# Performance work log

Measured on AMD Instinct MI355X. Metric: run time of the kernel, lower is better.

Reference implementation:

```python
import jax, jax.numpy as jnp
import numpy as np

L = 6      # layers (enc and dec)
D = 512    # d_model
H = 8      # heads
DK = D // H
F = 2048   # dim_feedforward
B = 8
S = 512    # src len
T = 512    # tgt len
NEG = -1e9


def setup_inputs() -> dict:
    key = jax.random.key(0)
    ks = jax.random.split(key, 64)
    it = iter(ks)
    def w(shape, scale=0.02):
        return jax.random.normal(next(it), shape, dtype=jnp.float32) * scale
    inp = {}
    inp['src'] = jax.random.normal(next(it), (B, S, D), dtype=jnp.float32)
    inp['tgt'] = jax.random.normal(next(it), (B, T, D), dtype=jnp.float32)
    inp['tgt_mask'] = jnp.where(jnp.triu(jnp.ones((T, T), bool), 1), jnp.float32(NEG), jnp.float32(0.0))
    # encoder params (stacked over L layers)
    inp['enc_Wq'] = w((L, H, D, DK)); inp['enc_Wk'] = w((L, H, D, DK)); inp['enc_Wv'] = w((L, H, D, DK))
    inp['enc_Wo'] = w((L, D, D))
    inp['enc_ln1_a'] = jnp.ones((L, D)); inp['enc_ln1_b'] = jnp.zeros((L, D))
    inp['enc_W1'] = w((L, D, F)); inp['enc_b1'] = jnp.zeros((L, F))
    inp['enc_W2'] = w((L, F, D)); inp['enc_b2'] = jnp.zeros((L, D))
    inp['enc_ln2_a'] = jnp.ones((L, D)); inp['enc_ln2_b'] = jnp.zeros((L, D))
    # decoder params
    inp['dec_sWq'] = w((L, H, D, DK)); inp['dec_sWk'] = w((L, H, D, DK)); inp['dec_sWv'] = w((L, H, D, DK))
    inp['dec_sWo'] = w((L, D, D))
    inp['dec_ln1_a'] = jnp.ones((L, D)); inp['dec_ln1_b'] = jnp.zeros((L, D))
    inp['dec_cWq'] = w((L, H, D, DK)); inp['dec_cWk'] = w((L, H, D, DK)); inp['dec_cWv'] = w((L, H, D, DK))
    inp['dec_cWo'] = w((L, D, D))
    inp['dec_ln2_a'] = jnp.ones((L, D)); inp['dec_ln2_b'] = jnp.zeros((L, D))
    inp['dec_W1'] = w((L, D, F)); inp['dec_b1'] = jnp.zeros((L, F))
    inp['dec_W2'] = w((L, F, D)); inp['dec_b2'] = jnp.zeros((L, D))
    inp['dec_ln3_a'] = jnp.ones((L, D)); inp['dec_ln3_b'] = jnp.zeros((L, D))
    return inp


def layernorm(x, a, b):
    # faithful to the torch module: unbiased std (ddof=1) and eps added to std
    mean = x.mean(-1, keepdims=True)
    std = jnp.std(x, axis=-1, keepdims=True, ddof=1)
    return a * (x - mean) / (std + 1e-6) + b


def mha(qx, kx, vx, Wq, Wk, Wv, Wo, mask):
    # Wq/Wk/Wv: [H, D, dk] (per-head torch loop fused into one batched einsum)
    q = jnp.einsum('bsd,hdk->bhsk', qx, Wq)
    k = jnp.einsum('bsd,hdk->bhsk', kx, Wk)
    v = jnp.einsum('bsd,hdk->bhsk', vx, Wv)
    scores = jnp.einsum('bhqk,bhmk->bhqm', q, k) / np.float32(np.sqrt(Wq.shape[-1]))
    if mask is not None:
        scores = scores + mask  # [T,T] broadcasts over batch and heads
    attn = jax.nn.softmax(scores, axis=-1)
    o = jnp.einsum('bhqm,bhmk->bhqk', attn, v)
    b_, h_, s_, k_ = o.shape
    o = o.transpose(0, 2, 1, 3).reshape(b_, s_, h_ * k_)  # concat heads
    return o @ Wo


def ffn(x, W1, b1, W2, b2):
    return jnp.maximum(x @ W1 + b1, 0.0) @ W2 + b2


def reference(src, tgt, tgt_mask,
              enc_Wq, enc_Wk, enc_Wv, enc_Wo, enc_ln1_a, enc_ln1_b,
              enc_W1, enc_b1, enc_W2, enc_b2, enc_ln2_a, enc_ln2_b,
              dec_sWq, dec_sWk, dec_sWv, dec_sWo, dec_ln1_a, dec_ln1_b,
              dec_cWq, dec_cWk, dec_cWv, dec_cWo, dec_ln2_a, dec_ln2_b,
              dec_W1, dec_b1, dec_W2, dec_b2, dec_ln3_a, dec_ln3_b):
    # encoder
    x = src
    for i in range(L):
        h = x + mha(x, x, x, enc_Wq[i], enc_Wk[i], enc_Wv[i], enc_Wo[i], None)
        x = layernorm(h, enc_ln1_a[i], enc_ln1_b[i])
        h = x + ffn(x, enc_W1[i], enc_b1[i], enc_W2[i], enc_b2[i])
        x = layernorm(h, enc_ln2_a[i], enc_ln2_b[i])
    memory = x
    # decoder
    y = tgt
    for i in range(L):
        h = y + mha(y, y, y, dec_sWq[i], dec_sWk[i], dec_sWv[i], dec_sWo[i], tgt_mask)
        y = layernorm(h, dec_ln1_a[i], dec_ln1_b[i])
        h = y + mha(y, memory, memory, dec_cWq[i], dec_cWk[i], dec_cWv[i], dec_cWo[i], None)
        y = layernorm(h, dec_ln2_a[i], dec_ln2_b[i])
        h = y + ffn(y, dec_W1[i], dec_b1[i], dec_W2[i], dec_b2[i])
        y = layernorm(h, dec_ln3_a[i], dec_ln3_b[i])
    return y
```

## Files before the change

### kernel.cpp

```cpp
#include <hip/hip_runtime.h>
#include <hip/hip_bf16.h>

typedef unsigned short u16;
typedef __hip_bfloat16 hbf;
typedef __bf16 bf16x8 __attribute__((ext_vector_type(8)));
typedef float f32x4 __attribute__((ext_vector_type(4)));

#define LL 6
#define DD 512
#define HH 8
#define DKK 64
#define FF 2048
#define BB 8
#define SS 512

#define GLL(gp, lp)                                                        \
  __builtin_amdgcn_global_load_lds(                                        \
      (const __attribute__((address_space(1))) void*)(gp),                 \
      (__attribute__((address_space(3))) void*)(lp), 16, 0, 0)

__global__ __launch_bounds__(256) void cvt_k(const float* __restrict__ x,
                                             hbf* __restrict__ y, int n) {
  for (int i = (blockIdx.x * 256 + threadIdx.x) * 4; i < n; i += gridDim.x * 1024) {
    float4 v = *(const float4*)(x + i);
    y[i] = __float2bfloat16(v.x);
    y[i + 1] = __float2bfloat16(v.y);
    y[i + 2] = __float2bfloat16(v.z);
    y[i + 3] = __float2bfloat16(v.w);
  }
}

__global__ __launch_bounds__(256) void transpose_k(const float* __restrict__ src,
                                                   hbf* __restrict__ dst, int R, int C) {
  __shared__ hbf tile[64][65];
  const int b = blockIdx.z;
  src += (size_t)b * R * C;
  dst += (size_t)b * R * C;
  int c0 = blockIdx.x * 64, r0 = blockIdx.y * 64;
  int tx = threadIdx.x & 63;
  int ty = threadIdx.x >> 6;
#pragma unroll
  for (int i = 0; i < 16; i++) {
    int r = ty + i * 4;
    tile[r][tx] = __float2bfloat16(src[(size_t)(r0 + r) * C + c0 + tx]);
  }
  __syncthreads();
#pragma unroll
  for (int i = 0; i < 16; i++) {
    int r = ty + i * 4;
    dst[(size_t)(c0 + r) * R + r0 + tx] = tile[tx][r];
  }
}

__global__ __launch_bounds__(256) void transpose_qkv_k(const float* __restrict__ Wq,
                                                       const float* __restrict__ Wk,
                                                       const float* __restrict__ Wv,
                                                       hbf* __restrict__ dst) {
  __shared__ hbf tile[64][65];
  const int z = blockIdx.z;
  const int l = z / 24, r = z - l * 24;
  const int zw = r >> 3, h = r & 7;
  const float* src =
      (zw == 0 ? Wq : (zw == 1 ? Wk : Wv)) + ((size_t)l * HH + h) * DD * DKK;
  const int r0 = blockIdx.y * 64;
  const int tx = threadIdx.x & 63, ty = threadIdx.x >> 6;
#pragma unroll
  for (int i = 0; i < 16; i++) {
    int rr = ty + i * 4;
    tile[rr][tx] = __float2bfloat16(src[(size_t)(r0 + rr) * DKK + tx]);
  }
  __syncthreads();
  hbf* d = dst + (size_t)l * 3 * DD * DD + ((size_t)zw * 512 + h * 64) * DD + r0;
#pragma unroll
  for (int i = 0; i < 16; i++) {
    int rr = ty + i * 4;
    d[(size_t)rr * DD + tx] = tile[tx][rr];
  }
}

template <int BM, int MODE, int SPLITK>
__global__ __launch_bounds__(128) void gemm_nt(
    const u16* __restrict__ A, const u16* __restrict__ Bm, void* __restrict__ Cout,
    void* __restrict__ C2, void* __restrict__ C3,
    const float* __restrict__ bias, const hbf* __restrict__ res,
    int M, int N, int K, int lda, int ldb, int ldc, int ncoloff,
    long sAo, long sAi, long sBo, long sBi, long sCo, long sCi, int inner, float scale,
    const u16* __restrict__ A2) {
  constexpr int BN = 64, BK = 64;
  constexpr int AM = BM / 32;
  constexpr int NCA = BM / 16;
  constexpr int WR = BM / 2;
  __shared__ u16 As[2][BM * BK];
  __shared__ u16 Bs[2][BN * BK];

  int bxx = blockIdx.x, byy = blockIdx.y;
  {
    const int gx = gridDim.x, gy = gridDim.y;
    const int f = byy * gx + bxx;
    const int st = gy >> 3;
    const int rem = f >> 3;
    byy = (f & 7) * st + rem % st;
    bxx = rem / st;
  }

  int g = blockIdx.z;
  int ks = 0;
  if (SPLITK > 1) {
    ks = g;
    g = 0;
  }
  int outer = g / inner, inr = g - outer * inner;
  A += outer * sAo + inr * sAi;
  Bm += outer * sBo + inr * sBi;

  const int tid = threadIdx.x;
  const int m0 = byy * BM, n0 = (bxx + ncoloff) * BN;
  const int wave = tid >> 6, lane = tid & 63;
  const int m16 = lane & 15, quad = lane >> 4;
  const int l8 = lane & 7, ld8 = lane >> 3;
  const int scol = (l8 ^ ld8) << 3;

  const u16* Asel = (MODE == 4 && n0 >= 512) ? A2 : A;
  const u16* Ab = Asel + (size_t)m0 * lda;
  const u16* Bb = Bm + (size_t)n0 * ldb;

  f32x4 acc[AM][4] = {};

  const int kbeg = ks * (K / SPLITK);
  const int nt = (K / SPLITK) / BK;

  auto stage = [&](int b, int k0) {
#pragma unroll
    for (int c = 0; c < NCA; c++) {
      const int ch = wave * NCA + c;
      const int row = ch * 8 + ld8;
      GLL(Ab + (size_t)row * lda + k0 + scol, &As[b][ch * 512]);
    }
#pragma unroll
    for (int c = 0; c < 4; c++) {
      const int ch = wave * 4 + c;
      const int row = ch * 8 + ld8;
      GLL(Bb + (size_t)row * ldb + k0 + scol, &Bs[b][ch * 512]);
    }
  };

  stage(0, kbeg);
  __syncthreads();
  for (int t = 0; t < nt; t++) {
    if (t + 1 < nt) stage((t + 1) & 1, kbeg + (t + 1) * BK);
    const int cb = t & 1;
#pragma unroll
    for (int kc = 0; kc < 2; kc++) {
      bf16x8 af[AM], bfv[4];
      const int sw = (((kc << 2) | quad) ^ (m16 & 7)) << 3;
#pragma unroll
      for (int i = 0; i < AM; i++)
        af[i] = *(const bf16x8*)(&As[cb][(wave * WR + i * 16 + m16) * 64 + sw]);
#pragma unroll
      for (int j = 0; j < 4; j++)
        bfv[j] = *(const bf16x8*)(&Bs[cb][(j * 16 + m16) * 64 + sw]);
#pragma unroll
      for (int i = 0; i < AM; i++)
#pragma unroll
        for (int j = 0; j < 4; j++)
          acc[i][j] = __builtin_amdgcn_mfma_f32_16x16x32_bf16(af[i], bfv[j], acc[i][j], 0, 0, 0);
    }
    __syncthreads();
  }

#pragma unroll
  for (int i = 0; i < AM; i++) {
#pragma unroll
    for (int j = 0; j < 4; j++) {
      const int col = n0 + j * 16 + m16;
      const int rowb = m0 + wave * WR + i * 16 + quad * 4;
#pragma unroll
      for (int r = 0; r < 4; r++) {
        const int row = rowb + r;
        float v = acc[i][j][r] * scale;
        if (MODE == 0) {
          hbf* C = (hbf*)Cout + outer * sCo + inr * sCi;
          C[(size_t)row * ldc + col] = __float2bfloat16(v);
        } else if (MODE == 2) {
          float* C = (float*)((SPLITK > 1 && ks == 1) ? C2 : Cout);
          C += outer * sCo + inr * sCi;
          if (SPLITK == 1 || ks == 0) {
            if (bias) v += bias[col];
            if (res) v += __bfloat162float(res[(size_t)row * ldc + col]);
          }
          C[(size_t)row * ldc + col] = v;
        } else if (MODE == 3) {
          hbf* C = (hbf*)Cout + outer * sCo + inr * sCi;
          v += bias[col];
          C[(size_t)row * ldc + col] = __float2bfloat16(fmaxf(v, 0.0f));
        } else if (MODE == 4) {
          const int b = row >> 9, s = row & 511;
          const int which = col >> 9, h = (col >> 6) & 7, dk = col & 63;
          const int bh = (b << 3) + h;
          if (which == 0)
            ((hbf*)Cout)[((size_t)bh * SS + s) * DKK + dk] = __float2bfloat16(v * 0.125f);
          else if (which == 1)
            ((hbf*)C2)[((size_t)bh * SS + s) * DKK + dk] = __float2bfloat16(v);
          else
            ((hbf*)C3)[((size_t)bh * DKK + dk) * SS + s] = __float2bfloat16(v);
        }
      }
    }
  }
}

__global__ __launch_bounds__(256) void flash_k(const u16* __restrict__ Q,
                                               const u16* __restrict__ Kb,
                                               const u16* __restrict__ Vt,
                                               hbf* __restrict__ O, int causal) {
  __shared__ u16 Qs[32][72];
  __shared__ u16 Ks[128 * 72];
  __shared__ u16 Ss[32][520];
  const int bh = blockIdx.y;
  const int q0 = blockIdx.x * 32;
  const int b = bh >> 3, h = bh & 7;
  const int tid = threadIdx.x;
  const int wave = tid >> 6, lane = tid & 63;
  const int m16 = lane & 15, quad = lane >> 4;
  const int rg = (wave >> 1) * 16;
  const int chf = wave & 1;

  const u16* Qp = Q + ((size_t)bh * SS + q0) * DKK;
  const u16* Kp = Kb + (size_t)bh * SS * DKK;
  const u16* Vp = Vt + (size_t)bh * DKK * SS;

  const int ktmax = causal ? ((q0 + 31) >> 7) + 1 : 4;

  {
    int row = tid >> 3, ch = (tid & 7) << 3;
    *(float4*)(&Qs[row][ch]) = *(const float4*)(Qp + (size_t)row * DKK + ch);
  }

  for (int kt = 0; kt < ktmax; kt++) {
    if (kt > 0) __syncthreads();
#pragma unroll
    for (int p = 0; p < 4; p++) {
      int idx = p * 256 + tid;
      int row = idx >> 3, ch = (idx & 7) << 3;
      *(float4*)(&Ks[row * 72 + ch]) =
          *(const float4*)(Kp + (size_t)(kt * 128 + row) * DKK + ch);
    }
    __syncthreads();
#pragma unroll
    for (int ct = 0; ct < 4; ct++) {
      f32x4 s{};
#pragma unroll
      for (int kc = 0; kc < 2; kc++) {
        bf16x8 a = *(const bf16x8*)(&Qs[rg + m16][kc * 32 + quad * 8]);
        bf16x8 bv =
            *(const bf16x8*)(&Ks[(chf * 64 + ct * 16 + m16) * 72 + kc * 32 + quad * 8]);
        s = __builtin_amdgcn_mfma_f32_16x16x32_bf16(a, bv, s, 0, 0, 0);
      }
      const int colb = kt * 128 + chf * 64 + ct * 16 + m16;
#pragma unroll
      for (int r = 0; r < 4; r++)
        *((hbf*)&Ss[rg + quad * 4 + r][colb]) = __float2bfloat16(s[r]);
    }
  }
  __syncthreads();

#pragma unroll
  for (int rr = 0; rr < 8; rr++) {
    const int r = wave * 8 + rr;
    const int gr = q0 + r;
    float v[8];
#pragma unroll
    for (int i = 0; i < 8; i++) {
      const int col = lane + i * 64;
      v[i] = __bfloat162float(((const hbf*)Ss[r])[col]);
      if (causal && col > gr) v[i] = -1e30f;
    }
    float m = v[0];
#pragma unroll
    for (int i = 1; i < 8; i++) m = fmaxf(m, v[i]);
#pragma unroll
    for (int off = 1; off < 64; off <<= 1) m = fmaxf(m, __shfl_xor(m, off));
    float e[8], s = 0.f;
#pragma unroll
    for (int i = 0; i < 8; i++) {
      e[i] = __expf(v[i] - m);
      s += e[i];
    }
#pragma unroll
    for (int off = 1; off < 64; off <<= 1) s += __shfl_xor(s, off);
    const float inv = 1.0f / s;
#pragma unroll
    for (int i = 0; i < 8; i++)
      ((hbf*)Ss[r])[lane + i * 64] = __float2bfloat16(e[i] * inv);
  }
  __syncthreads();

  f32x4 o[2] = {};
  u16* Vs = Ks;
  for (int vt = 0; vt < ktmax; vt++) {
    if (vt > 0) __syncthreads();
#pragma unroll
    for (int p = 0; p < 4; p++) {
      int idx = p * 256 + tid;
      int row = idx >> 4, ch = (idx & 15) << 3;
      *(float4*)(&Vs[row * 136 + ch]) =
          *(const float4*)(Vp + (size_t)row * SS + vt * 128 + ch);
    }
    __syncthreads();
#pragma unroll
    for (int kc = 0; kc < 4; kc++) {
      bf16x8 a = *(const bf16x8*)(&Ss[rg + m16][vt * 128 + kc * 32 + quad * 8]);
#pragma unroll
      for (int dt = 0; dt < 2; dt++) {
        bf16x8 bv =
            *(const bf16x8*)(&Vs[(chf * 32 + dt * 16 + m16) * 136 + kc * 32 + quad * 8]);
        o[dt] = __builtin_amdgcn_mfma_f32_16x16x32_bf16(a, bv, o[dt], 0, 0, 0);
      }
    }
  }
#pragma unroll
  for (int dt = 0; dt < 2; dt++) {
    const int d = h * 64 + chf * 32 + dt * 16 + m16;
#pragma unroll
    for (int r = 0; r < 4; r++) {
      const int row = q0 + rg + quad * 4 + r;
      O[(size_t)b * SS * DD + (size_t)row * DD + d] = __float2bfloat16(o[dt][r]);
    }
  }
}

template <typename T>
__global__ __launch_bounds__(256) void layernorm_k(const float* __restrict__ X,
                                                   const float* __restrict__ X2,
                                                   const float* __restrict__ ga,
                                                   const float* __restrict__ gb,
                                                   T* __restrict__ out, int Dn) {
  const int row = blockIdx.x;
  X += (size_t)row * Dn;
  X2 += (size_t)row * Dn;
  out += (size_t)row * Dn;
  const int t = threadIdx.x;
  float2 xv = *(const float2*)(X + 2 * t);
  float2 x2 = *(const float2*)(X2 + 2 * t);
  xv.x += x2.x;
  xv.y += x2.y;
  float s = xv.x + xv.y, ss = xv.x * xv.x + xv.y * xv.y;
#pragma unroll
  for (int off = 32; off > 0; off >>= 1) {
    s += __shfl_down(s, off);
    ss += __shfl_down(ss, off);
  }
  __shared__ float sm[8];
  __shared__ float smean, sinv;
  const int wv = t >> 6, ln = t & 63;
  if (ln == 0) {
    sm[wv] = s;
    sm[4 + wv] = ss;
  }
  __syncthreads();
  if (t == 0) {
    float S1 = sm[0] + sm[1] + sm[2] + sm[3];
    float S2 = sm[4] + sm[5] + sm[6] + sm[7];
    float mean = S1 / Dn;
    float var = (S2 - S1 * mean) / (Dn - 1);
    var = fmaxf(var, 0.0f);
    smean = mean;
    sinv = 1.0f / (sqrtf(var) + 1e-6f);
  }
  __syncthreads();
  const float mean = smean, inv = sinv;
  float o0 = ga[2 * t] * (xv.x - mean) * inv + gb[2 * t];
  float o1 = ga[2 * t + 1] * (xv.y - mean) * inv + gb[2 * t + 1];
  if constexpr (sizeof(T) == 2) {
    out[2 * t] = (T)__float2bfloat16(o0);
    out[2 * t + 1] = (T)__float2bfloat16(o1);
  } else {
    out[2 * t] = o0;
    out[2 * t + 1] = o1;
  }
}

extern "C" void kernel_launch(void* const* d_in, const int* in_sizes, int n_in,
                              void* d_out, int out_size, void* d_ws, size_t ws_size,
                              hipStream_t stream) {
  (void)in_sizes; (void)n_in; (void)out_size;
  const float* src = (const float*)d_in[0];
  const float* tgt = (const float*)d_in[1];
  const float* eWq = (const float*)d_in[3];
  const float* eWk = (const float*)d_in[4];
  const float* eWv = (const float*)d_in[5];
  const float* eWo = (const float*)d_in[6];
  const float* eln1a = (const float*)d_in[7];
  const float* eln1b = (const float*)d_in[8];
  const float* eW1 = (const float*)d_in[9];
  const float* eb1 = (const float*)d_in[10];
  const float* eW2 = (const float*)d_in[11];
  const float* eb2 = (const float*)d_in[12];
  const float* eln2a = (const float*)d_in[13];
  const float* eln2b = (const float*)d_in[14];
  const float* sWq = (const float*)d_in[15];
  const float* sWk = (const float*)d_in[16];
  const float* sWv = (const float*)d_in[17];
  const float* sWo = (const float*)d_in[18];
  const float* dln1a = (const float*)d_in[19];
  const float* dln1b = (const float*)d_in[20];
  const float* cWq = (const float*)d_in[21];
  const float* cWk = (const float*)d_in[22];
  const float* cWv = (const float*)d_in[23];
  const float* cWo = (const float*)d_in[24];
  const float* dln2a = (const float*)d_in[25];
  const float* dln2b = (const float*)d_in[26];
  const float* dW1 = (const float*)d_in[27];
  const float* db1 = (const float*)d_in[28];
  const float* dW2 = (const float*)d_in[29];
  const float* db2 = (const float*)d_in[30];
  const float* dln3a = (const float*)d_in[31];
  const float* dln3b = (const float*)d_in[32];

  const size_t MB = 1024 * 1024;
  char* ws = (char*)d_ws;
  const size_t QKV_L = (size_t)3 * DD * DD;
  const size_t WO_L = (size_t)DD * DD;
  const size_t WF_L = (size_t)DD * FF;
  const bool preT = ws_size >= 150 * MB;

  hbf *qkvT_all = nullptr, *woT_all = nullptr, *w1T_all = nullptr, *w2T_all = nullptr;
  hbf *wqkvS = nullptr, *woS = nullptr, *w1S = nullptr, *w2S = nullptr;
  char* actb;
  if (preT) {
    qkvT_all = (hbf*)(ws);
    woT_all = (hbf*)(ws + 28311552);
    w1T_all = (hbf*)(ws + 37748736);
    w2T_all = (hbf*)(ws + 62914560);
    actb = ws + 84 * MB;
  } else {
    if (ws_size < 72 * MB) return;
    wqkvS = (hbf*)(ws);
    woS = (hbf*)(ws + 2 * MB);
    w1S = (hbf*)(ws + 2 * MB + 512 * 1024);
    w2S = (hbf*)(ws + 4 * MB + 512 * 1024);
    actb = ws + 7 * MB;
  }
  hbf* sbuf = (hbf*)(actb);
  u16* xbuf = (u16*)(actb + 4 * MB);
  hbf* tbuf = (hbf*)(actb + 8 * MB);
  u16* ybuf = (u16*)(actb + 12 * MB);
  u16* qbuf = (u16*)(actb + 16 * MB);
  u16* kbuf = (u16*)(actb + 20 * MB);
  u16* vtb = (u16*)(actb + 24 * MB);
  u16* obuf = (u16*)(actb + 28 * MB);
  u16* ffnh = (u16*)(actb + 32 * MB);
  float* projf = (float*)(actb + 48 * MB);
  float* projf2 = (float*)(actb + 56 * MB);

  const size_t WQL = (size_t)HH * DD * DKK;
  const size_t WOL = (size_t)DD * DD;
  const size_t WFL = (size_t)DD * FF;

  if (preT) {
    transpose_qkv_k<<<dim3(1, 8, LL * 24), dim3(256), 0, stream>>>(eWq, eWk, eWv, qkvT_all);
    transpose_qkv_k<<<dim3(1, 8, LL * 24), dim3(256), 0, stream>>>(sWq, sWk, sWv,
                                                                   qkvT_all + LL * QKV_L);
    transpose_qkv_k<<<dim3(1, 8, LL * 24), dim3(256), 0, stream>>>(
        cWq, cWk, cWv, qkvT_all + 2 * LL * QKV_L);
    transpose_k<<<dim3(8, 8, LL), dim3(256), 0, stream>>>(eWo, woT_all, DD, DD);
    transpose_k<<<dim3(8, 8, LL), dim3(256), 0, stream>>>(sWo, woT_all + LL * WO_L, DD, DD);
    transpose_k<<<dim3(8, 8, LL), dim3(256), 0, stream>>>(cWo, woT_all + 2 * LL * WO_L, DD, DD);
    transpose_k<<<dim3(32, 8, LL), dim3(256), 0, stream>>>(eW1, w1T_all, DD, FF);
    transpose_k<<<dim3(32, 8, LL), dim3(256), 0, stream>>>(dW1, w1T_all + LL * WF_L, DD, FF);
    transpose_k<<<dim3(8, 32, LL), dim3(256), 0, stream>>>(eW2, w2T_all, FF, DD);
    transpose_k<<<dim3(8, 32, LL), dim3(256), 0, stream>>>(dW2, w2T_all + LL * WF_L, FF, DD);
  }

  auto attention = [&](const u16* qin, const u16* kvin, const hbf* qkvTl, const hbf* woTl,
                       const u16* resid, int causal) {
    gemm_nt<128, 4, 1><<<dim3(24, 32, 1), dim3(128), 0, stream>>>(
        qin, (const u16*)qkvTl, qbuf, kbuf, vtb, nullptr, nullptr,
        BB * SS, 3 * DD, DD, DD, DD, 0, 0,
        0, 0, 0, 0, 0, 0, 1, 1.f, kvin);
    flash_k<<<dim3(16, 64), dim3(256), 0, stream>>>(qbuf, kbuf, vtb, (hbf*)obuf, causal);
    gemm_nt<64, 2, 2><<<dim3(8, 64, 2), dim3(128), 0, stream>>>(
        obuf, (const u16*)woTl, projf, projf2, nullptr, nullptr, (const hbf*)resid,
        BB * SS, DD, DD, DD, DD, DD, 0,
        0, 0, 0, 0, 0, 0, 1, 1.f, nullptr);
  };

  auto ffn = [&](const u16* xin, const hbf* w1Tl, const float* b1l, const hbf* w2Tl,
                 const float* b2l) {
    gemm_nt<128, 3, 1><<<dim3(32, 32, 1), dim3(128), 0, stream>>>(
        xin, (const u16*)w1Tl, ffnh, nullptr, nullptr, b1l, nullptr,
        BB * SS, FF, DD, DD, DD, FF, 0,
        0, 0, 0, 0, 0, 0, 1, 1.f, nullptr);
    gemm_nt<64, 2, 2><<<dim3(8, 64, 2), dim3(128), 0, stream>>>(
        ffnh, (const u16*)w2Tl, projf, projf2, nullptr, b2l, (const hbf*)xin,
        BB * SS, DD, FF, FF, FF, DD, 0,
        0, 0, 0, 0, 0, 0, 1, 1.f, nullptr);
  };

  auto lnb = [&](const float* X, const float* a, const float* b, u16* out) {
    layernorm_k<hbf><<<dim3(BB * SS), dim3(256), 0, stream>>>(X, projf2, a, b, (hbf*)out, DD);
  };

  cvt_k<<<dim3(2048), dim3(256), 0, stream>>>(src, sbuf, BB * SS * DD);
  cvt_k<<<dim3(2048), dim3(256), 0, stream>>>(tgt, tbuf, BB * SS * DD);

  const u16* cur = (const u16*)sbuf;
  for (int l = 0; l < LL; l++) {
    const hbf *qkvTl, *woTl, *w1Tl, *w2Tl;
    if (preT) {
      qkvTl = qkvT_all + (size_t)l * QKV_L;
      woTl = woT_all + (size_t)l * WO_L;
      w1Tl = w1T_all + (size_t)l * WF_L;
      w2Tl = w2T_all + (size_t)l * WF_L;
    } else {
      transpose_qkv_k<<<dim3(1, 8, 24), dim3(256), 0, stream>>>(
          eWq + l * WQL, eWk + l * WQL, eWv + l * WQL, wqkvS);
      transpose_k<<<dim3(8, 8, 1), dim3(256), 0, stream>>>(eWo + l * WOL, woS, DD, DD);
      qkvTl = wqkvS;
      woTl = woS;
    }
    attention(cur, cur, qkvTl, woTl, cur, 0);
    lnb(projf, eln1a + l * DD, eln1b + l * DD, xbuf);
    if (!preT) {
      transpose_k<<<dim3(32, 8, 1), dim3(256), 0, stream>>>(eW1 + l * WFL, w1S, DD, FF);
      transpose_k<<<dim3(8, 32, 1), dim3(256), 0, stream>>>(eW2 + l * WFL, w2S, FF, DD);
      w1Tl = w1S;
      w2Tl = w2S;
    }
    ffn(xbuf, w1Tl, eb1 + l * FF, w2Tl, eb2 + l * DD);
    lnb(projf, eln2a + l * DD, eln2b + l * DD, xbuf);
    cur = xbuf;
  }
  const u16* mem = cur;
  const u16* yc = (const u16*)tbuf;
  for (int l = 0; l < LL; l++) {
    const hbf *sqkvTl, *swoTl, *cqkvTl, *cwoTl, *w1Tl, *w2Tl;
    if (preT) {
      sqkvTl = qkvT_all + ((size_t)LL + l) * QKV_L;
      swoTl = woT_all + ((size_t)LL + l) * WO_L;
      cqkvTl = qkvT_all + ((size_t)2 * LL + l) * QKV_L;
      cwoTl = woT_all + ((size_t)2 * LL + l) * WO_L;
      w1Tl = w1T_all + ((size_t)LL + l) * WF_L;
      w2Tl = w2T_all + ((size_t)LL + l) * WF_L;
    }
    if (!preT) {
      transpose_qkv_k<<<dim3(1, 8, 24), dim3(256), 0, stream>>>(
          sWq + l * WQL, sWk + l * WQL, sWv + l * WQL, wqkvS);
      transpose_k<<<dim3(8, 8, 1), dim3(256), 0, stream>>>(sWo + l * WOL, woS, DD, DD);
      sqkvTl = wqkvS;
      swoTl = woS;
    }
    attention(yc, yc, sqkvTl, swoTl, yc, 1);
    lnb(projf, dln1a + l * DD, dln1b + l * DD, ybuf);
    yc = ybuf;
    if (!preT) {
      transpose_qkv_k<<<dim3(1, 8, 24), dim3(256), 0, stream>>>(
          cWq + l * WQL, cWk + l * WQL, cWv + l * WQL, wqkvS);
      transpose_k<<<dim3(8, 8, 1), dim3(256), 0, stream>>>(cWo + l * WOL, woS, DD, DD);
      cqkvTl = wqkvS;
      cwoTl = woS;
    }
    attention(yc, mem, cqkvTl, cwoTl, yc, 0);
    lnb(projf, dln2a + l * DD, dln2b + l * DD, ybuf);
    if (!preT) {
      transpose_k<<<dim3(32, 8, 1), dim3(256), 0, stream>>>(dW1 + l * WFL, w1S, DD, FF);
      transpose_k<<<dim3(8, 32, 1), dim3(256), 0, stream>>>(dW2 + l * WFL, w2S, FF, DD);
      w1Tl = w1S;
      w2Tl = w2S;
    }
    ffn(ybuf, w1Tl, db1 + l * FF, w2Tl, db2 + l * DD);
    if (l == LL - 1) {
      layernorm_k<float><<<dim3(BB * SS), dim3(256), 0, stream>>>(
          projf, projf2, dln3a + l * DD, dln3b + l * DD, (float*)d_out, DD);
    } else {
      lnb(projf, dln3a + l * DD, dln3b + l * DD, ybuf);
      yc = ybuf;
    }
  }
}
```

Measured before the change: 2.112 ms.

## Fuse output-projection and FFN2 GEMMs with residual add and layernorm

Adds a gemm_ln kernel in which each block computes a 16-row by 512-column output tile, adds bias and the bf16 residual, then does the row layernorm in registers and LDS before writing bf16 or fp32. It replaces the split-K GEMM that wrote two fp32 partial buffers, plus the separate layernorm kernel, for the Wo and W2 projections. This removes the fp32 round trips and one launch per sublayer. The trade-off is that every block streams the whole weight matrix for only 16 rows, giving low weight reuse, about 132KB of LDS per block and a grid of 256 blocks.

```diff
diff --git a/kernel.cpp b/kernel.cpp
--- a/kernel.cpp
+++ b/kernel.cpp
@@ -209,6 +209,122 @@
   }
 }
 
+template <int OUTF32>
+__global__ __launch_bounds__(256) void gemm_ln(
+    const u16* __restrict__ A, const u16* __restrict__ Bm,
+    const float* __restrict__ bias, const hbf* __restrict__ res,
+    const float* __restrict__ ga, const float* __restrict__ gb,
+    void* __restrict__ out, int K) {
+  __shared__ u16 Bs[2][512 * 64];
+  __shared__ u16 As[2][16 * 64];
+  __shared__ float sred1[4][16], sred2[4][16];
+  __shared__ float smean[16], sinv[16];
+
+  const int tid = threadIdx.x;
+  const int wave = tid >> 6, lane = tid & 63;
+  const int m16 = lane & 15, quad = lane >> 4;
+  const int l8 = lane & 7, ld8 = lane >> 3;
+  const int scol = (l8 ^ ld8) << 3;
+  const int m0 = blockIdx.x * 16;
+  const int wn = wave * 128;
+
+  const u16* Ab = A + (size_t)m0 * K;
+  f32x4 acc[8] = {};
+
+  const int nt = K / 64;
+  auto stage = [&](int b, int k0) {
+#pragma unroll
+    for (int c = 0; c < 16; c++) {
+      const int ch = wave * 16 + c;
+      GLL(Bm + (size_t)(ch * 8 + ld8) * K + k0 + scol, &Bs[b][ch * 512]);
+    }
+    if (wave == 3) {
+#pragma unroll
+      for (int c = 0; c < 2; c++)
+        GLL(Ab + (size_t)(c * 8 + ld8) * K + k0 + scol, &As[b][c * 512]);
+    }
+  };
+
+  stage(0, 0);
+  __syncthreads();
+  for (int t = 0; t < nt; t++) {
+    if (t + 1 < nt) stage((t + 1) & 1, (t + 1) * 64);
+    const int cb = t & 1;
+#pragma unroll
+    for (int kc = 0; kc < 2; kc++) {
+      const int sw = (((kc << 2) | quad) ^ (m16 & 7)) << 3;
+      bf16x8 af = *(const bf16x8*)(&As[cb][m16 * 64 + sw]);
+#pragma unroll
+      for (int j = 0; j < 8; j++) {
+        bf16x8 bv = *(const bf16x8*)(&Bs[cb][(wn + j * 16 + m16) * 64 + sw]);
+        acc[j] = __builtin_amdgcn_mfma_f32_16x16x32_bf16(af, bv, acc[j], 0, 0, 0);
+      }
+    }
+    __syncthreads();
+  }
+
+  const int rowl = quad * 4;
+#pragma unroll
+  for (int j = 0; j < 8; j++) {
+    const int col = wn + j * 16 + m16;
+    const float bi = bias ? bias[col] : 0.f;
+#pragma unroll
+    for (int r = 0; r < 4; r++) {
+      float x = acc[j][r] + bi;
+      x += __bfloat162float(res[(size_t)(m0 + rowl + r) * 512 + col]);
+      acc[j][r] = x;
+    }
+  }
+#pragma unroll
+  for (int r = 0; r < 4; r++) {
+    float s1 = 0.f, s2 = 0.f;
+#pragma unroll
+    for (int j = 0; j < 8; j++) {
+      s1 += acc[j][r];
+      s2 += acc[j][r] * acc[j][r];
+    }
+#pragma unroll
+    for (int off = 1; off < 16; off <<= 1) {
+      s1 += __shfl_xor(s1, off);
+      s2 += __shfl_xor(s2, off);
+    }
+    if (m16 == 0) {
+      sred1[wave][rowl + r] = s1;
+      sred2[wave][rowl + r] = s2;
+    }
+  }
+  __syncthreads();
+  if (tid < 16) {
+    float S1 = sred1[0][tid] + sred1[1][tid] + sred1[2][tid] + sred1[3][tid];
+    float S2 = sred2[0][tid] + sred2[1][tid] + sred2[2][tid] + sred2[3][tid];
+    float mean = S1 / 512.f;
+    float var = fmaxf((S2 - S1 * mean) / 511.f, 0.f);
+    smean[tid] = mean;
+    sinv[tid] = 1.f / (sqrtf(var) + 1e-6f);
+  }
+  __syncthreads();
+  float mn[4], iv[4];
+#pragma unroll
+  for (int r = 0; r < 4; r++) {
+    mn[r] = smean[rowl + r];
+    iv[r] = sinv[rowl + r];
+  }
+#pragma unroll
+  for (int j = 0; j < 8; j++) {
+    const int col = wn + j * 16 + m16;
+    const float g = ga[col], be = gb[col];
+#pragma unroll
+    for (int r = 0; r < 4; r++) {
+      const size_t idx = (size_t)(m0 + rowl + r) * 512 + col;
+      float o = g * (acc[j][r] - mn[r]) * iv[r] + be;
+      if (OUTF32)
+        ((float*)out)[idx] = o;
+      else
+        ((hbf*)out)[idx] = __float2bfloat16(o);
+    }
+  }
+}
+
 __global__ __launch_bounds__(256) void flash_k(const u16* __restrict__ Q,
                                                const u16* __restrict__ Kb,
                                                const u16* __restrict__ Vt,
@@ -326,57 +442,6 @@
       const int row = q0 + rg + quad * 4 + r;
       O[(size_t)b * SS * DD + (size_t)row * DD + d] = __float2bfloat16(o[dt][r]);
     }
-  }
-}
-
-template <typename T>
-__global__ __launch_bounds__(256) void layernorm_k(const float* __restrict__ X,
-                                                   const float* __restrict__ X2,
-                                                   const float* __restrict__ ga,
-                                                   const float* __restrict__ gb,
-                                                   T* __restrict__ out, int Dn) {
-  const int row = blockIdx.x;
-  X += (size_t)row * Dn;
-  X2 += (size_t)row * Dn;
-  out += (size_t)row * Dn;
-  const int t = threadIdx.x;
-  float2 xv = *(const float2*)(X + 2 * t);
-  float2 x2 = *(const float2*)(X2 + 2 * t);
-  xv.x += x2.x;
-  xv.y += x2.y;
-  float s = xv.x + xv.y, ss = xv.x * xv.x + xv.y * xv.y;
-#pragma unroll
-  for (int off = 32; off > 0; off >>= 1) {
-    s += __shfl_down(s, off);
-    ss += __shfl_down(ss, off);
-  }
-  __shared__ float sm[8];
-  __shared__ float smean, sinv;
-  const int wv = t >> 6, ln = t & 63;
-  if (ln == 0) {
-    sm[wv] = s;
-    sm[4 + wv] = ss;
-  }
-  __syncthreads();
-  if (t == 0) {
-    float S1 = sm[0] + sm[1] + sm[2] + sm[3];
-    float S2 = sm[4] + sm[5] + sm[6] + sm[7];
-    float mean = S1 / Dn;
-    float var = (S2 - S1 * mean) / (Dn - 1);
-    var = fmaxf(var, 0.0f);
-    smean = mean;
-    sinv = 1.0f / (sqrtf(var) + 1e-6f);
-  }
-  __syncthreads();
-  const float mean = smean, inv = sinv;
-  float o0 = ga[2 * t] * (xv.x - mean) * inv + gb[2 * t];
-  float o1 = ga[2 * t + 1] * (xv.y - mean) * inv + gb[2 * t + 1];
-  if constexpr (sizeof(T) == 2) {
-    out[2 * t] = (T)__float2bfloat16(o0);
-    out[2 * t + 1] = (T)__float2bfloat16(o1);
-  } else {
-    out[2 * t] = o0;
-    out[2 * t + 1] = o1;
   }
 }
 
@@ -450,8 +515,6 @@
   u16* vtb = (u16*)(actb + 24 * MB);
   u16* obuf = (u16*)(actb + 28 * MB);
   u16* ffnh = (u16*)(actb + 32 * MB);
-  float* projf = (float*)(actb + 48 * MB);
-  float* projf2 = (float*)(actb + 56 * MB);
 
   const size_t WQL = (size_t)HH * DD * DKK;
   const size_t WOL = (size_t)DD * DD;
@@ -473,32 +536,30 @@
   }
 
   auto attention = [&](const u16* qin, const u16* kvin, const hbf* qkvTl, const hbf* woTl,
-                       const u16* resid, int causal) {
+                       const u16* resid, int causal, const float* la, const float* lb,
+                       void* outb) {
     gemm_nt<128, 4, 1><<<dim3(24, 32, 1), dim3(128), 0, stream>>>(
         qin, (const u16*)qkvTl, qbuf, kbuf, vtb, nullptr, nullptr,
         BB * SS, 3 * DD, DD, DD, DD, 0, 0,
         0, 0, 0, 0, 0, 0, 1, 1.f, kvin);
     flash_k<<<dim3(16, 64), dim3(256), 0, stream>>>(qbuf, kbuf, vtb, (hbf*)obuf, causal);
-    gemm_nt<64, 2, 2><<<dim3(8, 64, 2), dim3(128), 0, stream>>>(
-        obuf, (const u16*)woTl, projf, projf2, nullptr, nullptr, (const hbf*)resid,
-        BB * SS, DD, DD, DD, DD, DD, 0,
-        0, 0, 0, 0, 0, 0, 1, 1.f, nullptr);
+    gemm_ln<0><<<dim3(256), dim3(256), 0, stream>>>(
+        obuf, (const u16*)woTl, nullptr, (const hbf*)resid, la, lb, outb, DD);
   };
 
   auto ffn = [&](const u16* xin, const hbf* w1Tl, const float* b1l, const hbf* w2Tl,
-                 const float* b2l) {
+                 const float* b2l, const float* la, const float* lb, void* outb,
+                 bool f32o) {
     gemm_nt<128, 3, 1><<<dim3(32, 32, 1), dim3(128), 0, stream>>>(
         xin, (const u16*)w1Tl, ffnh, nullptr, nullptr, b1l, nullptr,
         BB * SS, FF, DD, DD, DD, FF, 0,
         0, 0, 0, 0, 0, 0, 1, 1.f, nullptr);
-    gemm_nt<64, 2, 2><<<dim3(8, 64, 2), dim3(128), 0, stream>>>(
-        ffnh, (const u16*)w2Tl, projf, projf2, nullptr, b2l, (const hbf*)xin,
-        BB * SS, DD, FF, FF, FF, DD, 0,
-        0, 0, 0, 0, 0, 0, 1, 1.f, nullptr);
-  };
-
-  auto lnb = [&](const float* X, const float* a, const float* b, u16* out) {
-    layernorm_k<hbf><<<dim3(BB * SS), dim3(256), 0, stream>>>(X, projf2, a, b, (hbf*)out, DD);
+    if (f32o)
+      gemm_ln<1><<<dim3(256), dim3(256), 0, stream>>>(
+          ffnh, (const u16*)w2Tl, b2l, (const hbf*)xin, la, lb, outb, FF);
+    else
+      gemm_ln<0><<<dim3(256), dim3(256), 0, stream>>>(
+          ffnh, (const u16*)w2Tl, b2l, (const hbf*)xin, la, lb, outb, FF);
   };
 
   cvt_k<<<dim3(2048), dim3(256), 0, stream>>>(src, sbuf, BB * SS * DD);
@@ -519,16 +580,15 @@
       qkvTl = wqkvS;
       woTl = woS;
     }
-    attention(cur, cur, qkvTl, woTl, cur, 0);
-    lnb(projf, eln1a + l * DD, eln1b + l * DD, xbuf);
+    attention(cur, cur, qkvTl, woTl, cur, 0, eln1a + l * DD, eln1b + l * DD, xbuf);
     if (!preT) {
       transpose_k<<<dim3(32, 8, 1), dim3(256), 0, stream>>>(eW1 + l * WFL, w1S, DD, FF);
       transpose_k<<<dim3(8, 32, 1), dim3(256), 0, stream>>>(eW2 + l * WFL, w2S, FF, DD);
       w1Tl = w1S;
       w2Tl = w2S;
     }
-    ffn(xbuf, w1Tl, eb1 + l * FF, w2Tl, eb2 + l * DD);
-    lnb(projf, eln2a + l * DD, eln2b + l * DD, xbuf);
+    ffn(xbuf, w1Tl, eb1 + l * FF, w2Tl, eb2 + l * DD, eln2a + l * DD, eln2b + l * DD,
+        xbuf, false);
     cur = xbuf;
   }
   const u16* mem = cur;
@@ -550,8 +610,7 @@
       sqkvTl = wqkvS;
       swoTl = woS;
     }
-    attention(yc, yc, sqkvTl, swoTl, yc, 1);
-    lnb(projf, dln1a + l * DD, dln1b + l * DD, ybuf);
+    attention(yc, yc, sqkvTl, swoTl, yc, 1, dln1a + l * DD, dln1b + l * DD, ybuf);
     yc = ybuf;
     if (!preT) {
       transpose_qkv_k<<<dim3(1, 8, 24), dim3(256), 0, stream>>>(
@@ -560,20 +619,19 @@
       cqkvTl = wqkvS;
       cwoTl = woS;
     }
-    attention(yc, mem, cqkvTl, cwoTl, yc, 0);
-    lnb(projf, dln2a + l * DD, dln2b + l * DD, ybuf);
+    attention(yc, mem, cqkvTl, cwoTl, yc, 0, dln2a + l * DD, dln2b + l * DD, ybuf);
     if (!preT) {
       transpose_k<<<dim3(32, 8, 1), dim3(256), 0, stream>>>(dW1 + l * WFL, w1S, DD, FF);
       transpose_k<<<dim3(8, 32, 1), dim3(256), 0, stream>>>(dW2 + l * WFL, w2S, FF, DD);
       w1Tl = w1S;
       w2Tl = w2S;
     }
-    ffn(ybuf, w1Tl, db1 + l * FF, w2Tl, db2 + l * DD);
     if (l == LL - 1) {
-      layernorm_k<float><<<dim3(BB * SS), dim3(256), 0, stream>>>(
-          projf, projf2, dln3a + l * DD, dln3b + l * DD, (float*)d_out, DD);
+      ffn(ybuf, w1Tl, db1 + l * FF, w2Tl, db2 + l * DD, dln3a + l * DD, dln3b + l * DD,
+          d_out, true);
     } else {
-      lnb(projf, dln3a + l * DD, dln3b + l * DD, ybuf);
+      ffn(ybuf, w1Tl, db1 + l * FF, w2Tl, db2 + l * DD, dln3a + l * DD, dln3b + l * DD,
+          ybuf, false);
       yc = ybuf;
     }
   }
```

Measured after the change: 2.120 ms. No clear change (+0.4%).

## Double-buffer K/V tiles in flash kernel and split FFN down-proj 4-way

Applied to the files above, without the earlier changes.

The flash attention kernel now double-buffers K and V tiles in shared memory. The next tile is loaded into registers while MFMAs run on the current one, and the V prefetch is issued during softmax. The FFN second GEMM goes from 2-way to 4-way split-K, with four fp32 partial buffers that the layernorm kernel sums. This targets global-load latency in attention and the low block count of the K=2048 down-projection, at the cost of more shared memory per block and extra fp32 partial-buffer traffic.

```diff
diff --git a/kernel.cpp b/kernel.cpp
--- a/kernel.cpp
+++ b/kernel.cpp
@@ -182,9 +182,16 @@
           hbf* C = (hbf*)Cout + outer * sCo + inr * sCi;
           C[(size_t)row * ldc + col] = __float2bfloat16(v);
         } else if (MODE == 2) {
-          float* C = (float*)((SPLITK > 1 && ks == 1) ? C2 : Cout);
+          float* C;
+          if (SPLITK == 4)
+            C = (ks == 0) ? (float*)Cout
+                          : (ks == 1) ? (float*)C2
+                                      : (ks == 2) ? (float*)C3
+                                                  : (float*)(void*)const_cast<u16*>(A2);
+          else
+            C = (float*)((SPLITK > 1 && ks == 1) ? C2 : Cout);
           C += outer * sCo + inr * sCi;
-          if (SPLITK == 1 || ks == 0) {
+          if (ks == 0) {
             if (bias) v += bias[col];
             if (res) v += __bfloat162float(res[(size_t)row * ldc + col]);
           }
@@ -214,7 +221,7 @@
                                                const u16* __restrict__ Vt,
                                                hbf* __restrict__ O, int causal) {
   __shared__ u16 Qs[32][72];
-  __shared__ u16 Ks[128 * 72];
+  __shared__ u16 KV[2][128 * 72];
   __shared__ u16 Ss[32][520];
   const int bh = blockIdx.y;
   const int q0 = blockIdx.x * 32;
@@ -231,21 +238,52 @@
 
   const int ktmax = causal ? ((q0 + 31) >> 7) + 1 : 4;
 
-  {
-    int row = tid >> 3, ch = (tid & 7) << 3;
-    *(float4*)(&Qs[row][ch]) = *(const float4*)(Qp + (size_t)row * DKK + ch);
-  }
-
-  for (int kt = 0; kt < ktmax; kt++) {
-    if (kt > 0) __syncthreads();
+  float4 reg[4];
+  auto kload = [&](int kt) {
 #pragma unroll
     for (int p = 0; p < 4; p++) {
       int idx = p * 256 + tid;
       int row = idx >> 3, ch = (idx & 7) << 3;
-      *(float4*)(&Ks[row * 72 + ch]) =
-          *(const float4*)(Kp + (size_t)(kt * 128 + row) * DKK + ch);
-    }
-    __syncthreads();
+      reg[p] = *(const float4*)(Kp + (size_t)(kt * 128 + row) * DKK + ch);
+    }
+  };
+  auto kstore = [&](int bb) {
+#pragma unroll
+    for (int p = 0; p < 4; p++) {
+      int idx = p * 256 + tid;
+      int row = idx >> 3, ch = (idx & 7) << 3;
+      *(float4*)(&KV[bb][row * 72 + ch]) = reg[p];
+    }
+  };
+  auto vload = [&](int vt) {
+#pragma unroll
+    for (int p = 0; p < 4; p++) {
+      int idx = p * 256 + tid;
+      int row = idx >> 4, ch = (idx & 15) << 3;
+      reg[p] = *(const float4*)(Vp + (size_t)row * SS + vt * 128 + ch);
+    }
+  };
+  auto vstore = [&](int bb) {
+#pragma unroll
+    for (int p = 0; p < 4; p++) {
+      int idx = p * 256 + tid;
+      int row = idx >> 4, ch = (idx & 15) << 3;
+      *(float4*)(&KV[bb][row * 136 + ch]) = reg[p];
+    }
+  };
+
+  {
+    int row = tid >> 3, ch = (tid & 7) << 3;
+    float4 qv = *(const float4*)(Qp + (size_t)row * DKK + ch);
+    kload(0);
+    *(float4*)(&Qs[row][ch]) = qv;
+    kstore(0);
+  }
+  __syncthreads();
+
+  for (int kt = 0; kt < ktmax; kt++) {
+    if (kt + 1 < ktmax) kload(kt + 1);
+    const u16* Ksb = KV[kt & 1];
 #pragma unroll
     for (int ct = 0; ct < 4; ct++) {
       f32x4 s{};
@@ -253,7 +291,7 @@
       for (int kc = 0; kc < 2; kc++) {
         bf16x8 a = *(const bf16x8*)(&Qs[rg + m16][kc * 32 + quad * 8]);
         bf16x8 bv =
-            *(const bf16x8*)(&Ks[(chf * 64 + ct * 16 + m16) * 72 + kc * 32 + quad * 8]);
+            *(const bf16x8*)(&Ksb[(chf * 64 + ct * 16 + m16) * 72 + kc * 32 + quad * 8]);
         s = __builtin_amdgcn_mfma_f32_16x16x32_bf16(a, bv, s, 0, 0, 0);
       }
       const int colb = kt * 128 + chf * 64 + ct * 16 + m16;
@@ -261,8 +299,14 @@
       for (int r = 0; r < 4; r++)
         *((hbf*)&Ss[rg + quad * 4 + r][colb]) = __float2bfloat16(s[r]);
     }
-  }
-  __syncthreads();
+    if (kt + 1 < ktmax) {
+      kstore((kt + 1) & 1);
+      __syncthreads();
+    }
+  }
+  __syncthreads();
+
+  vload(0);
 
 #pragma unroll
   for (int rr = 0; rr < 8; rr++) {
@@ -293,29 +337,26 @@
     for (int i = 0; i < 8; i++)
       ((hbf*)Ss[r])[lane + i * 64] = __float2bfloat16(e[i] * inv);
   }
+  vstore(0);
   __syncthreads();
 
   f32x4 o[2] = {};
-  u16* Vs = Ks;
   for (int vt = 0; vt < ktmax; vt++) {
-    if (vt > 0) __syncthreads();
-#pragma unroll
-    for (int p = 0; p < 4; p++) {
-      int idx = p * 256 + tid;
-      int row = idx >> 4, ch = (idx & 15) << 3;
-      *(float4*)(&Vs[row * 136 + ch]) =
-          *(const float4*)(Vp + (size_t)row * SS + vt * 128 + ch);
-    }
-    __syncthreads();
+    if (vt + 1 < ktmax) vload(vt + 1);
+    const u16* Vsb = KV[vt & 1];
 #pragma unroll
     for (int kc = 0; kc < 4; kc++) {
       bf16x8 a = *(const bf16x8*)(&Ss[rg + m16][vt * 128 + kc * 32 + quad * 8]);
 #pragma unroll
       for (int dt = 0; dt < 2; dt++) {
         bf16x8 bv =
-            *(const bf16x8*)(&Vs[(chf * 32 + dt * 16 + m16) * 136 + kc * 32 + quad * 8]);
+            *(const bf16x8*)(&Vsb[(chf * 32 + dt * 16 + m16) * 136 + kc * 32 + quad * 8]);
         o[dt] = __builtin_amdgcn_mfma_f32_16x16x32_bf16(a, bv, o[dt], 0, 0, 0);
       }
+    }
+    if (vt + 1 < ktmax) {
+      vstore((vt + 1) & 1);
+      __syncthreads();
     }
   }
 #pragma unroll
@@ -329,9 +370,11 @@
   }
 }
 
-template <typename T>
+template <typename T, int P>
 __global__ __launch_bounds__(256) void layernorm_k(const float* __restrict__ X,
                                                    const float* __restrict__ X2,
+                                                   const float* __restrict__ X3,
+                                                   const float* __restrict__ X4,
                                                    const float* __restrict__ ga,
                                                    const float* __restrict__ gb,
                                                    T* __restrict__ out, int Dn) {
@@ -344,6 +387,12 @@
   float2 x2 = *(const float2*)(X2 + 2 * t);
   xv.x += x2.x;
   xv.y += x2.y;
+  if (P == 4) {
+    float2 x3 = *(const float2*)(X3 + (size_t)row * Dn + 2 * t);
+    float2 x4 = *(const float2*)(X4 + (size_t)row * Dn + 2 * t);
+    xv.x += x3.x + x4.x;
+    xv.y += x3.y + x4.y;
+  }
   float s = xv.x + xv.y, ss = xv.x * xv.x + xv.y * xv.y;
 #pragma unroll
   for (int off = 32; off > 0; off >>= 1) {
@@ -452,6 +501,8 @@
   u16* ffnh = (u16*)(actb + 32 * MB);
   float* projf = (float*)(actb + 48 * MB);
   float* projf2 = (float*)(actb + 56 * MB);
+  float* projf3 = (float*)(actb + 16 * MB);
+  float* projf4 = (float*)(actb + 24 * MB);
 
   const size_t WQL = (size_t)HH * DD * DKK;
   const size_t WOL = (size_t)DD * DD;
@@ -473,7 +524,8 @@
   }
 
   auto attention = [&](const u16* qin, const u16* kvin, const hbf* qkvTl, const hbf* woTl,
-                       const u16* resid, int causal) {
+                       const u16* resid, int causal, const float* la, const float* lb,
+                       u16* outb) {
     gemm_nt<128, 4, 1><<<dim3(24, 32, 1), dim3(128), 0, stream>>>(
         qin, (const u16*)qkvTl, qbuf, kbuf, vtb, nullptr, nullptr,
         BB * SS, 3 * DD, DD, DD, DD, 0, 0,
@@ -483,22 +535,27 @@
         obuf, (const u16*)woTl, projf, projf2, nullptr, nullptr, (const hbf*)resid,
         BB * SS, DD, DD, DD, DD, DD, 0,
         0, 0, 0, 0, 0, 0, 1, 1.f, nullptr);
+    layernorm_k<hbf, 2><<<dim3(BB * SS), dim3(256), 0, stream>>>(
+        projf, projf2, nullptr, nullptr, la, lb, (hbf*)outb, DD);
   };
 
   auto ffn = [&](const u16* xin, const hbf* w1Tl, const float* b1l, const hbf* w2Tl,
-                 const float* b2l) {
+                 const float* b2l, const float* la, const float* lb, void* outb,
+                 bool f32o) {
     gemm_nt<128, 3, 1><<<dim3(32, 32, 1), dim3(128), 0, stream>>>(
         xin, (const u16*)w1Tl, ffnh, nullptr, nullptr, b1l, nullptr,
         BB * SS, FF, DD, DD, DD, FF, 0,
         0, 0, 0, 0, 0, 0, 1, 1.f, nullptr);
-    gemm_nt<64, 2, 2><<<dim3(8, 64, 2), dim3(128), 0, stream>>>(
-        ffnh, (const u16*)w2Tl, projf, projf2, nullptr, b2l, (const hbf*)xin,
+    gemm_nt<64, 2, 4><<<dim3(8, 64, 4), dim3(128), 0, stream>>>(
+        ffnh, (const u16*)w2Tl, projf, projf2, projf3, b2l, (const hbf*)xin,
         BB * SS, DD, FF, FF, FF, DD, 0,
-        0, 0, 0, 0, 0, 0, 1, 1.f, nullptr);
-  };
-
-  auto lnb = [&](const float* X, const float* a, const float* b, u16* out) {
-    layernorm_k<hbf><<<dim3(BB * SS), dim3(256), 0, stream>>>(X, projf2, a, b, (hbf*)out, DD);
+        0, 0, 0, 0, 0, 0, 1, 1.f, (const u16*)projf4);
+    if (f32o)
+      layernorm_k<float, 4><<<dim3(BB * SS), dim3(256), 0, stream>>>(
+          projf, projf2, projf3, projf4, la, lb, (float*)outb, DD);
+    else
+      layernorm_k<hbf, 4><<<dim3(BB * SS), dim3(256), 0, stream>>>(
+          projf, projf2, projf3, projf4, la, lb, (hbf*)outb, DD);
   };
 
   cvt_k<<<dim3(2048), dim3(256), 0, stream>>>(src, sbuf, BB * SS * DD);
@@ -519,16 +576,15 @@
       qkvTl = wqkvS;
       woTl = woS;
     }
-    attention(cur, cur, qkvTl, woTl, cur, 0);
-    lnb(projf, eln1a + l * DD, eln1b + l * DD, xbuf);
+    attention(cur, cur, qkvTl, woTl, cur, 0, eln1a + l * DD, eln1b + l * DD, xbuf);
     if (!preT) {
       transpose_k<<<dim3(32, 8, 1), dim3(256), 0, stream>>>(eW1 + l * WFL, w1S, DD, FF);
       transpose_k<<<dim3(8, 32, 1), dim3(256), 0, stream>>>(eW2 + l * WFL, w2S, FF, DD);
       w1Tl = w1S;
       w2Tl = w2S;
     }
-    ffn(xbuf, w1Tl, eb1 + l * FF, w2Tl, eb2 + l * DD);
-    lnb(projf, eln2a + l * DD, eln2b + l * DD, xbuf);
+    ffn(xbuf, w1Tl, eb1 + l * FF, w2Tl, eb2 + l * DD, eln2a + l * DD, eln2b + l * DD,
+        xbuf, false);
     cur = xbuf;
   }
   const u16* mem = cur;
@@ -550,8 +606,7 @@
       sqkvTl = wqkvS;
       swoTl = woS;
     }
-    attention(yc, yc, sqkvTl, swoTl, yc, 1);
-    lnb(projf, dln1a + l * DD, dln1b + l * DD, ybuf);
+    attention(yc, yc, sqkvTl, swoTl, yc, 1, dln1a + l * DD, dln1b + l * DD, ybuf);
     yc = ybuf;
     if (!preT) {
       transpose_qkv_k<<<dim3(1, 8, 24), dim3(256), 0, stream>>>(
@@ -560,20 +615,19 @@
       cqkvTl = wqkvS;
       cwoTl = woS;
     }
-    attention(yc, mem, cqkvTl, cwoTl, yc, 0);
-    lnb(projf, dln2a + l * DD, dln2b + l * DD, ybuf);
+    attention(yc, mem, cqkvTl, cwoTl, yc, 0, dln2a + l * DD, dln2b + l * DD, ybuf);
     if (!preT) {
       transpose_k<<<dim3(32, 8, 1), dim3(256), 0, stream>>>(dW1 + l * WFL, w1S, DD, FF);
       transpose_k<<<dim3(8, 32, 1), dim3(256), 0, stream>>>(dW2 + l * WFL, w2S, FF, DD);
       w1Tl = w1S;
       w2Tl = w2S;
     }
-    ffn(ybuf, w1Tl, db1 + l * FF, w2Tl, db2 + l * DD);
     if (l == LL - 1) {
-      layernorm_k<float><<<dim3(BB * SS), dim3(256), 0, stream>>>(
-          projf, projf2, dln3a + l * DD, dln3b + l * DD, (float*)d_out, DD);
+      ffn(ybuf, w1Tl, db1 + l * FF, w2Tl, db2 + l * DD, dln3a + l * DD, dln3b + l * DD,
+          d_out, true);
     } else {
-      lnb(projf, dln3a + l * DD, dln3b + l * DD, ybuf);
+      ffn(ybuf, w1Tl, db1 + l * FF, w2Tl, db2 + l * DD, dln3a + l * DD, dln3b + l * DD,
+          ybuf, false);
       yc = ybuf;
     }
   }
```

Result: slower. 2.377 ms (+12.5%).
